# Optimization experiments

Hardware: AMD Instinct MI355X
Metric: run time of the kernel (lower is better)

Reference implementation:

```python
import jax, jax.numpy as jnp
import numpy as np

N = 2048        # nodes
IN_DIM = 128    # input feature dim
K = 8           # channels
D = 32          # per-channel dim (C_dim)
ITERS = 4       # routing iterations
BETA = 1.0      # attention temperature
EPS = 1e-12     # F.normalize eps


def l2norm(x):
    # F.normalize(x, dim=-1): x / max(||x||_2, eps)
    n = jnp.linalg.norm(x, axis=-1, keepdims=True)
    return x / jnp.maximum(n, EPS)


def setup_inputs() -> dict:
    key = jax.random.key(0)
    k1, k2, k3, k4 = jax.random.split(key, 4)
    adj = jax.random.randint(k1, (N, N), 0, 2, dtype=jnp.int32)
    features = jax.random.normal(k2, (N, IN_DIM), dtype=jnp.float32)
    # parameters initialized ~ N(0,1) as in init_parameters
    W = jax.random.normal(k3, (K, IN_DIM, D), dtype=jnp.float32)
    b = jax.random.normal(k4, (K, D), dtype=jnp.float32)
    return {"adj": adj, "features": features, "W": W, "b": b}


def reference(adj, features, W, b):
    mask = (adj > 0)[None, :, :]                         # [1, N, N]
    # per-channel projection + row L2 normalize -> Z: [K, N, D]
    Z = l2norm(jnp.einsum('nd,kdc->knc', features, W) + b[:, None, :])
    for _ in range(ITERS):
        # per-channel masked attention scores [K, N, N]
        att = jnp.einsum('knc,kmc->knm', Z, Z)
        att = jnp.where(mask, att, 0.0) / BETA
        # softmax across channels (dim=2 in torch after cat == K axis here)
        att = jax.nn.softmax(att, axis=0)
        att = jnp.where(mask, att, 0.0)
        # weighted aggregate + residual + L2 normalize
        Z = l2norm(Z + jnp.einsum('knm,kmc->knc', att, Z))
    # concat channels along feature dim -> [N, K*D]
    return jnp.transpose(Z, (1, 0, 2)).reshape(N, K * D)
```

## Files before the change

kernel.cpp:

```cpp
#include <hip/hip_runtime.h>
#include <hip/hip_bf16.h>
#include <hip/hip_fp16.h>
#include <hip/hip_cooperative_groups.h>

namespace cg = cooperative_groups;

#define NN 2048
#define KK 8
#define DD 32
#define ZSZ (KK * NN * DD)

#define TW(row, slot) (((row) << 4) + ((((slot) ^ (((row) >> 1) & 3))) << 2))
#define TW2(row, wo) (((row) << 4) + (((((wo) >> 2) ^ (((row) >> 1) & 3))) << 2) + ((wo) & 3))

typedef __attribute__((ext_vector_type(8))) short short8;
typedef __attribute__((ext_vector_type(4))) short short4v;
typedef __attribute__((ext_vector_type(4))) float f32x4;
typedef __attribute__((ext_vector_type(4))) unsigned int u32x4;

union UU { u32x4 q; short8 v; unsigned int u[4]; };
union U2 { uint2 q; short4v v; unsigned int u[2]; };

__device__ __forceinline__ unsigned int bfr(float x) {
  unsigned int u = __float_as_uint(x);
  return (u + 0x7fffu + ((u >> 16) & 1u)) >> 16;
}
__device__ __forceinline__ float bf2f(unsigned int h) {
  return __uint_as_float(h << 16);
}
__device__ __forceinline__ unsigned int packp(float a, float b) {
  union { __hip_bfloat162 h; unsigned int u; } cv;
  cv.h = __float22bfloat162_rn(make_float2(a, b));
  return cv.u;
}
__device__ __forceinline__ f32x4 MF(short8 a, short8 b, f32x4 c) {
  return __builtin_amdgcn_mfma_f32_16x16x32_bf16(a, b, c, 0, 0, 0);
}
__device__ __forceinline__ f32x4 MF16(short4v a, short4v b, f32x4 c) {
  return __builtin_amdgcn_mfma_f32_16x16x16bf16_1k(a, b, c, 0, 0, 0);
}
__device__ __forceinline__ short8 as_s8(u32x4 x) { UU u; u.q = x; return u.v; }

__global__ __launch_bounds__(256, 2) void mega_kernel(
    const float* feat, const float* W, const float* bias, const int* adj,
    unsigned short* Zghi, unsigned short* Zthi, unsigned int* mbits,
    __half* part, float* out) {
  __shared__ __align__(16) unsigned int lds[20480];
  cg::grid_group grid = cg::this_grid();
  const int bx = blockIdx.x;
  const int t = threadIdx.x;
  const int w = t >> 6;
  const int lane = t & 63;
  const int l15 = lane & 15;
  const int g = lane >> 4;

  unsigned int* Zg = (unsigned int*)Zghi;
  unsigned int* Zt = (unsigned int*)Zthi;

  {
    const int nb = bx * 4;
    const int k = t >> 5, c = t & 31;
    float* fsh = (float*)lds;
    if (t < 128) *(float4*)&fsh[4 * t] = *(const float4*)&feat[nb * 128 + 4 * t];
    float s[4];
#pragma unroll
    for (int j = 0; j < 4; ++j) s[j] = bias[k * DD + c];
    __syncthreads();
    const float* wp = W + (k * 128) * DD + c;
#pragma unroll 4
    for (int d = 0; d < 128; ++d) {
      float wv = wp[d * DD];
#pragma unroll
      for (int j = 0; j < 4; ++j) s[j] = fmaf(fsh[j * 128 + d], wv, s[j]);
    }
    unsigned int hi[4];
#pragma unroll
    for (int j = 0; j < 4; ++j) {
      float sq = s[j] * s[j];
#pragma unroll
      for (int off = 16; off > 0; off >>= 1) sq += __shfl_xor(sq, off, 32);
      float z = s[j] / fmaxf(sqrtf(sq), 1e-12f);
      hi[j] = bfr(z);
      Zghi[(k * NN + nb + j) * DD + c] = (unsigned short)hi[j];
    }
    *(uint2*)&Zthi[(size_t)k * DD * NN + (size_t)c * NN + nb] =
        make_uint2(hi[0] | (hi[1] << 16), hi[2] | (hi[3] << 16));

    const int base = bx * 8192 + t;
#pragma unroll
    for (int q = 0; q < 4; ++q) {
      int v[8];
#pragma unroll
      for (int r = 0; r < 8; ++r) v[r] = adj[base + 256 * (8 * q + r)];
#pragma unroll
      for (int r = 0; r < 8; ++r) {
        int idx = base + 256 * (8 * q + r);
        unsigned long long b = __ballot(v[r] > 0);
        if (lane == 0) mbits[idx >> 5] = (unsigned int)b;
        if (lane == 32) mbits[idx >> 5] = (unsigned int)(b >> 32);
      }
    }
  }
  grid.sync();

  const int nblk = (bx >> 3) & 31;
  const int chunk = (bx & 7) * 2 + (bx >> 8);
  const int nw = nblk * 64 + w * 16;
  const int mchunk = chunk * 128;
  const int sqd = t & 3;
  const int sr0 = t >> 2;

#pragma unroll 1
  for (int it = 0; it < 4; ++it) {
    {
      short8 A[KK];
#pragma unroll
      for (int k = 0; k < KK; ++k)
        A[k] = as_s8(*(const u32x4*)&Zg[(size_t)(k * NN + nw + l15) * 16 + 4 * g]);

      unsigned int mword[4];
      {
        uint4 m4 = *(const uint4*)&mbits[(size_t)(nw + l15) * 64 + (mchunk >> 5)];
        mword[0] = m4.x; mword[1] = m4.y; mword[2] = m4.z; mword[3] = m4.w;
      }

      f32x4 O[KK][2];
#pragma unroll
      for (int k = 0; k < KK; ++k)
#pragma unroll
        for (int ch = 0; ch < 2; ++ch) O[k][ch] = {0.0f, 0.0f, 0.0f, 0.0f};

      u32x4 Lgh[4], Lth[4];
      auto dl_g = [&](int mb) {
#pragma unroll
        for (int j = 0; j < 4; ++j) {
          int r = 64 * j + sr0;
          int k = r >> 5, rm = r & 31;
          Lgh[j] = *(const u32x4*)&Zg[(size_t)(k * NN + mb + rm) * 16 + 4 * sqd];
        }
      };
      auto wr_g = [&](int buf) {
#pragma unroll
        for (int j = 0; j < 4; ++j)
          *(u32x4*)&lds[buf * 4096 + TW(64 * j + sr0, sqd)] = Lgh[j];
      };
      auto dl_t = [&](int mb) {
#pragma unroll
        for (int j = 0; j < 4; ++j) {
          int r = 64 * j + sr0;
          int k = r >> 5, rm = r & 31;
          Lth[j] = *(const u32x4*)&Zt[(size_t)k * (NN * 16) + (size_t)rm * (NN / 2) + (mb >> 1) + 4 * sqd];
        }
      };
      auto wr_t = [&](int buf) {
#pragma unroll
        for (int j = 0; j < 4; ++j)
          *(u32x4*)&lds[12288 + buf * 4096 + TW(64 * j + sr0, sqd)] = Lth[j];
      };
      auto gram = [&](int gbuf, int sub, f32x4* S) {
#pragma unroll
        for (int k = 0; k < KK; ++k) {
          u32x4 bh = *(const u32x4*)&lds[gbuf * 4096 + TW(k * 32 + 16 * sub + l15, g)];
          f32x4 z = {0.0f, 0.0f, 0.0f, 0.0f};
          S[k] = MF(as_s8(bh), A[k], z);
        }
      };
      auto finish = [&](f32x4* S, int tbuf, int sub, unsigned int mw) {
#pragma unroll
        for (int r = 0; r < 4; ++r) {
          float e[KK];
          float sum = 0.0f;
#pragma unroll
          for (int k = 0; k < KK; ++k) { e[k] = __expf(S[k][r]); sum += e[k]; }
          float f = ((mw >> (16 * sub + 4 * g + r)) & 1u) ? __builtin_amdgcn_rcpf(sum) : 0.0f;
#pragma unroll
          for (int k = 0; k < KK; ++k) S[k][r] = e[k] * f;
        }
#pragma unroll
        for (int k = 0; k < KK; ++k) {
          U2 pa;
          pa.u[0] = packp(S[k][0], S[k][1]);
          pa.u[1] = packp(S[k][2], S[k][3]);
#pragma unroll
          for (int ch = 0; ch < 2; ++ch) {
            int row = k * 32 + 16 * ch + l15;
            U2 bv;
            bv.q = *(const uint2*)&lds[12288 + tbuf * 4096 + TW2(row, 8 * sub + 2 * g)];
            O[k][ch] = MF16(pa.v, bv.v, O[k][ch]);
          }
        }
      };

      dl_g(mchunk); wr_g(0);
      dl_g(mchunk + 32); wr_g(1);
      dl_t(mchunk); wr_t(0);
      dl_g(mchunk + 64);
      dl_t(mchunk + 32);
      __syncthreads();

      f32x4 Scur[KK], Snxt[KK];
      gram(0, 0, Scur);

#pragma unroll
      for (int st = 0; st < 4; ++st) {
        if (st + 2 < 4) wr_g((st + 2) % 3);
        if (st + 1 < 4) wr_t((st + 1) & 1);
        if (st + 3 < 4) dl_g(mchunk + (st + 3) * 32);
        if (st + 2 < 4) dl_t(mchunk + (st + 2) * 32);
        const unsigned int mw = mword[st];

        gram(st % 3, 1, Snxt);
        finish(Scur, st & 1, 0, mw);
        if (st + 1 < 4) gram((st + 1) % 3, 0, Scur);
        finish(Snxt, st & 1, 1, mw);
        __syncthreads();
      }

      __half* dst = part + (size_t)chunk * ZSZ;
#pragma unroll
      for (int k = 0; k < KK; ++k)
#pragma unroll
        for (int ch = 0; ch < 2; ++ch) {
          f32x4 o = O[k][ch];
#pragma unroll
          for (int r = 0; r < 4; ++r)
            dst[(size_t)(k * NN + nw + 4 * g + r) * DD + 16 * ch + l15] = __float2half_rn(o[r]);
        }
    }
    grid.sync();

    if (it < 3) {
      {
        unsigned int* T32 = lds;
        const int k = bx >> 6, mt = bx & 63;
        const int m0 = mt * 32;
        const int mloc = t >> 3, c4 = t & 7;
        const size_t idx = (size_t)(k * NN + m0 + mloc) * DD + 4 * c4;
        uint2 zb = *(const uint2*)&Zghi[idx];
        float4 v;
        v.x = bf2f(zb.x & 0xffffu);
        v.y = __uint_as_float(zb.x & 0xffff0000u);
        v.z = bf2f(zb.y & 0xffffu);
        v.w = __uint_as_float(zb.y & 0xffff0000u);
#pragma unroll
        for (int j = 0; j < 16; ++j) {
          const __half2* ph = (const __half2*)&part[(size_t)j * ZSZ + idx];
          float2 a = __half22float2(ph[0]);
          float2 bb = __half22float2(ph[1]);
          v.x += a.x; v.y += a.y; v.z += bb.x; v.w += bb.y;
        }
        float sq = v.x * v.x + v.y * v.y + v.z * v.z + v.w * v.w;
        sq += __shfl_xor(sq, 1, 8);
        sq += __shfl_xor(sq, 2, 8);
        sq += __shfl_xor(sq, 4, 8);
        const float sc = 1.0f / fmaxf(sqrtf(sq), 1e-12f);
        float z[4] = {v.x * sc, v.y * sc, v.z * sc, v.w * sc};
        unsigned int hi[4];
#pragma unroll
        for (int e = 0; e < 4; ++e) {
          hi[e] = bfr(z[e]);
          T32[(4 * c4 + e) * 37 + mloc] = hi[e];
        }
        *(uint2*)&Zghi[idx] = make_uint2(hi[0] | (hi[1] << 16), hi[2] | (hi[3] << 16));
        __syncthreads();
        const int cloc = t >> 3, m4i = t & 7;
        unsigned int o0 = T32[cloc * 37 + 4 * m4i + 0] | (T32[cloc * 37 + 4 * m4i + 1] << 16);
        unsigned int o1 = T32[cloc * 37 + 4 * m4i + 2] | (T32[cloc * 37 + 4 * m4i + 3] << 16);
        *(uint2*)&Zthi[(size_t)k * DD * NN + (size_t)cloc * NN + m0 + 4 * m4i] =
            make_uint2(o0, o1);
        __syncthreads();
      }
      grid.sync();
    }
  }

  {
    const int k = t >> 5, c = t & 31;
#pragma unroll
    for (int jj = 0; jj < 4; ++jj) {
      const int n = bx * 4 + jj;
      const size_t idx = (size_t)(k * NN + n) * DD + c;
      float v = bf2f((unsigned int)Zghi[idx]);
#pragma unroll
      for (int j = 0; j < 16; ++j) v += __half2float(part[(size_t)j * ZSZ + idx]);
      float sq = v * v;
#pragma unroll
      for (int off = 16; off > 0; off >>= 1) sq += __shfl_xor(sq, off, 32);
      out[n * (KK * DD) + t] = v / fmaxf(sqrtf(sq), 1e-12f);
    }
  }
}

__global__ __launch_bounds__(256) void pm_kernel(const float* __restrict__ feat,
                                                 const float* __restrict__ W,
                                                 const float* __restrict__ bias,
                                                 unsigned short* __restrict__ Zghi,
                                                 unsigned short* __restrict__ Zthi,
                                                 const int* __restrict__ adj,
                                                 unsigned int* __restrict__ mbits) {
  __shared__ float fsh[1024];
  const int t = threadIdx.x;
  if (blockIdx.x < 256) {
    const int nb = blockIdx.x * 8;
    const int k = t >> 5, c = t & 31;
    *(float4*)&fsh[4 * t] = *(const float4*)&feat[nb * 128 + 4 * t];
    float s[8];
#pragma unroll
    for (int j = 0; j < 8; ++j) s[j] = bias[k * DD + c];
    const float* w = W + (k * 128) * DD + c;
    __syncthreads();
#pragma unroll 4
    for (int d = 0; d < 128; ++d) {
      float wv = w[d * DD];
#pragma unroll
      for (int j = 0; j < 8; ++j) s[j] = fmaf(fsh[j * 128 + d], wv, s[j]);
    }
    unsigned int hi[8];
#pragma unroll
    for (int j = 0; j < 8; ++j) {
      float sq = s[j] * s[j];
#pragma unroll
      for (int off = 16; off > 0; off >>= 1) sq += __shfl_xor(sq, off, 32);
      float z = s[j] / fmaxf(sqrtf(sq), 1e-12f);
      hi[j] = bfr(z);
      Zghi[(k * NN + nb + j) * DD + c] = (unsigned short)hi[j];
    }
    uint4 tp = make_uint4(hi[0] | (hi[1] << 16), hi[2] | (hi[3] << 16),
                          hi[4] | (hi[5] << 16), hi[6] | (hi[7] << 16));
    *(uint4*)&Zthi[(size_t)k * DD * NN + (size_t)c * NN + nb] = tp;
  } else {
    const int base = (blockIdx.x - 256) * 1024 + t;
    const int lane = t & 63;
    int v[4];
#pragma unroll
    for (int rr = 0; rr < 4; ++rr) v[rr] = adj[base + 256 * rr];
#pragma unroll
    for (int rr = 0; rr < 4; ++rr) {
      int idx = base + 256 * rr;
      unsigned long long b = __ballot(v[rr] > 0);
      if (lane == 0) mbits[idx >> 5] = (unsigned int)b;
      if (lane == 32) mbits[idx >> 5] = (unsigned int)(b >> 32);
    }
  }
}

__global__ __launch_bounds__(256) void rp_kernel(const __half* __restrict__ part,
                                                 unsigned short* __restrict__ Zghi,
                                                 unsigned short* __restrict__ Zthi) {
  __shared__ unsigned int T32[32 * 37];
  const int t = threadIdx.x;
  const int k = blockIdx.x >> 6, mt = blockIdx.x & 63;
  const int m0 = mt * 32;
  const int mloc = t >> 3, c4 = t & 7;
  const size_t idx = (size_t)(k * NN + m0 + mloc) * DD + 4 * c4;
  uint2 zb = *(const uint2*)&Zghi[idx];
  float4 v;
  v.x = bf2f(zb.x & 0xffffu);
  v.y = __uint_as_float(zb.x & 0xffff0000u);
  v.z = bf2f(zb.y & 0xffffu);
  v.w = __uint_as_float(zb.y & 0xffff0000u);
#pragma unroll
  for (int j = 0; j < 16; ++j) {
    const __half2* ph = (const __half2*)&part[(size_t)j * ZSZ + idx];
    float2 a = __half22float2(ph[0]);
    float2 b = __half22float2(ph[1]);
    v.x += a.x; v.y += a.y; v.z += b.x; v.w += b.y;
  }
  float sq = v.x * v.x + v.y * v.y + v.z * v.z + v.w * v.w;
  sq += __shfl_xor(sq, 1, 8);
  sq += __shfl_xor(sq, 2, 8);
  sq += __shfl_xor(sq, 4, 8);
  const float sc = 1.0f / fmaxf(sqrtf(sq), 1e-12f);
  float z[4] = {v.x * sc, v.y * sc, v.z * sc, v.w * sc};
  unsigned int hi[4];
#pragma unroll
  for (int e = 0; e < 4; ++e) {
    hi[e] = bfr(z[e]);
    T32[(4 * c4 + e) * 37 + mloc] = hi[e];
  }
  *(uint2*)&Zghi[idx] = make_uint2(hi[0] | (hi[1] << 16), hi[2] | (hi[3] << 16));
  __syncthreads();
  const int cloc = t >> 3, m4 = t & 7;
  unsigned int o0 = T32[cloc * 37 + 4 * m4 + 0] | (T32[cloc * 37 + 4 * m4 + 1] << 16);
  unsigned int o1 = T32[cloc * 37 + 4 * m4 + 2] | (T32[cloc * 37 + 4 * m4 + 3] << 16);
  *(uint2*)&Zthi[(size_t)k * DD * NN + (size_t)cloc * NN + m0 + 4 * m4] = make_uint2(o0, o1);
}

__global__ __launch_bounds__(256, 2) void iter_kernel(const unsigned short* __restrict__ Zghi,
                                                      const unsigned short* __restrict__ Zthi,
                                                      const unsigned int* __restrict__ mbits,
                                                      __half* __restrict__ part) {
  __shared__ __align__(16) unsigned int lds[20480];
  const int t = threadIdx.x;
  const int w = t >> 6;
  const int lane = t & 63;
  const int l15 = lane & 15;
  const int g = lane >> 4;
  const int bx = blockIdx.x;
  const int nblk = (bx >> 3) & 31;
  const int chunk = (bx & 7) * 2 + (bx >> 8);
  const int nw = nblk * 64 + w * 16;
  const int mchunk = chunk * 128;

  const unsigned int* Zg = (const unsigned int*)Zghi;
  const unsigned int* Zt = (const unsigned int*)Zthi;

  short8 A[KK];
#pragma unroll
  for (int k = 0; k < KK; ++k)
    A[k] = as_s8(*(const u32x4*)&Zg[(size_t)(k * NN + nw + l15) * 16 + 4 * g]);

  unsigned int mword[4];
  {
    uint4 m4 = *(const uint4*)&mbits[(size_t)(nw + l15) * 64 + (mchunk >> 5)];
    mword[0] = m4.x; mword[1] = m4.y; mword[2] = m4.z; mword[3] = m4.w;
  }

  f32x4 O[KK][2];
#pragma unroll
  for (int k = 0; k < KK; ++k)
#pragma unroll
    for (int ch = 0; ch < 2; ++ch) O[k][ch] = {0.0f, 0.0f, 0.0f, 0.0f};

  const int sqd = t & 3;
  const int sr0 = t >> 2;

  u32x4 Lgh[4], Lth[4];
  auto dl_g = [&](int mb) {
#pragma unroll
    for (int j = 0; j < 4; ++j) {
      int r = 64 * j + sr0;
      int k = r >> 5, rm = r & 31;
      Lgh[j] = *(const u32x4*)&Zg[(size_t)(k * NN + mb + rm) * 16 + 4 * sqd];
    }
  };
  auto wr_g = [&](int buf) {
#pragma unroll
    for (int j = 0; j < 4; ++j)
      *(u32x4*)&lds[buf * 4096 + TW(64 * j + sr0, sqd)] = Lgh[j];
  };
  auto dl_t = [&](int mb) {
#pragma unroll
    for (int j = 0; j < 4; ++j) {
      int r = 64 * j + sr0;
      int k = r >> 5, rm = r & 31;
      Lth[j] = *(const u32x4*)&Zt[(size_t)k * (NN * 16) + (size_t)rm * (NN / 2) + (mb >> 1) + 4 * sqd];
    }
  };
  auto wr_t = [&](int buf) {
#pragma unroll
    for (int j = 0; j < 4; ++j)
      *(u32x4*)&lds[12288 + buf * 4096 + TW(64 * j + sr0, sqd)] = Lth[j];
  };
  auto gram = [&](int gbuf, int sub, f32x4* S) {
#pragma unroll
    for (int k = 0; k < KK; ++k) {
      u32x4 bh = *(const u32x4*)&lds[gbuf * 4096 + TW(k * 32 + 16 * sub + l15, g)];
      f32x4 z = {0.0f, 0.0f, 0.0f, 0.0f};
      S[k] = MF(as_s8(bh), A[k], z);
    }
  };
  auto finish = [&](f32x4* S, int tbuf, int sub, unsigned int mw) {
#pragma unroll
    for (int r = 0; r < 4; ++r) {
      float e[KK];
      float sum = 0.0f;
#pragma unroll
      for (int k = 0; k < KK; ++k) { e[k] = __expf(S[k][r]); sum += e[k]; }
      float f = ((mw >> (16 * sub + 4 * g + r)) & 1u) ? __builtin_amdgcn_rcpf(sum) : 0.0f;
#pragma unroll
      for (int k = 0; k < KK; ++k) S[k][r] = e[k] * f;
    }
#pragma unroll
    for (int k = 0; k < KK; ++k) {
      U2 pa;
      pa.u[0] = packp(S[k][0], S[k][1]);
      pa.u[1] = packp(S[k][2], S[k][3]);
#pragma unroll
      for (int ch = 0; ch < 2; ++ch) {
        int row = k * 32 + 16 * ch + l15;
        U2 bv;
        bv.q = *(const uint2*)&lds[12288 + tbuf * 4096 + TW2(row, 8 * sub + 2 * g)];
        O[k][ch] = MF16(pa.v, bv.v, O[k][ch]);
      }
    }
  };

  dl_g(mchunk); wr_g(0);
  dl_g(mchunk + 32); wr_g(1);
  dl_t(mchunk); wr_t(0);
  dl_g(mchunk + 64);
  dl_t(mchunk + 32);
  __syncthreads();

  f32x4 Scur[KK], Snxt[KK];
  gram(0, 0, Scur);

#pragma unroll
  for (int st = 0; st < 4; ++st) {
    if (st + 2 < 4) wr_g((st + 2) % 3);
    if (st + 1 < 4) wr_t((st + 1) & 1);
    if (st + 3 < 4) dl_g(mchunk + (st + 3) * 32);
    if (st + 2 < 4) dl_t(mchunk + (st + 2) * 32);
    const unsigned int mw = mword[st];

    gram(st % 3, 1, Snxt);
    finish(Scur, st & 1, 0, mw);
    if (st + 1 < 4) gram((st + 1) % 3, 0, Scur);
    finish(Snxt, st & 1, 1, mw);
    __syncthreads();
  }

  __half* dst = part + (size_t)chunk * ZSZ;
#pragma unroll
  for (int k = 0; k < KK; ++k)
#pragma unroll
    for (int ch = 0; ch < 2; ++ch) {
      f32x4 o = O[k][ch];
#pragma unroll
      for (int r = 0; r < 4; ++r)
        dst[(size_t)(k * NN + nw + 4 * g + r) * DD + 16 * ch + l15] = __float2half_rn(o[r]);
    }
}

__global__ __launch_bounds__(256) void ro_kernel(const unsigned short* __restrict__ Zghi,
                                                 const __half* __restrict__ part,
                                                 float* __restrict__ out) {
  const int n = blockIdx.x, t = threadIdx.x;
  const int k = t >> 5, c = t & 31;
  const size_t idx = (size_t)(k * NN + n) * DD + c;
  float v = bf2f((unsigned int)Zghi[idx]);
#pragma unroll
  for (int j = 0; j < 16; ++j) v += __half2float(part[(size_t)j * ZSZ + idx]);
  float sq = v * v;
#pragma unroll
  for (int off = 16; off > 0; off >>= 1) sq += __shfl_xor(sq, off, 32);
  out[n * (KK * DD) + t] = v / fmaxf(sqrtf(sq), 1e-12f);
}

extern "C" void kernel_launch(void* const* d_in, const int* in_sizes, int n_in,
                              void* d_out, int out_size, void* d_ws, size_t ws_size,
                              hipStream_t stream) {
  const int* adj = (const int*)d_in[0];
  const float* feat = (const float*)d_in[1];
  const float* W = (const float*)d_in[2];
  const float* b = (const float*)d_in[3];
  float* out = (float*)d_out;

  unsigned short* Zghi = (unsigned short*)d_ws;
  unsigned short* Zthi = Zghi + ZSZ;
  unsigned int* mbits = (unsigned int*)(Zthi + ZSZ);
  __half* part = (__half*)(mbits + NN * 64);

  bool coop_ok = false;
  int maxb = 0;
  if (hipOccupancyMaxActiveBlocksPerMultiprocessor(&maxb, mega_kernel, 256, 0) == hipSuccess &&
      maxb >= 2) {
    void* kargs[] = {(void*)&feat, (void*)&W, (void*)&b, (void*)&adj,
                     (void*)&Zghi, (void*)&Zthi, (void*)&mbits, (void*)&part, (void*)&out};
    if (hipLaunchCooperativeKernel((const void*)mega_kernel, dim3(512), dim3(256), kargs, 0,
                                   stream) == hipSuccess)
      coop_ok = true;
  }
  if (coop_ok) return;

  pm_kernel<<<256 + 4096, 256, 0, stream>>>(feat, W, b, Zghi, Zthi, adj, mbits);
  for (int it = 0; it < 4; ++it) {
    iter_kernel<<<512, 256, 0, stream>>>(Zghi, Zthi, mbits, part);
    if (it < 3)
      rp_kernel<<<512, 256, 0, stream>>>(part, Zghi, Zthi);
    else
      ro_kernel<<<NN, 256, 0, stream>>>(Zghi, part, out);
  }
}
```

Baseline: 182.1 us.

## Permute transposed Z layout so one 16-byte LDS read serves both sub-tiles

```diff
diff --git a/kernel.cpp b/kernel.cpp
--- a/kernel.cpp
+++ b/kernel.cpp
@@ -11,7 +11,6 @@
 #define ZSZ (KK * NN * DD)
 
 #define TW(row, slot) (((row) << 4) + ((((slot) ^ (((row) >> 1) & 3))) << 2))
-#define TW2(row, wo) (((row) << 4) + (((((wo) >> 2) ^ (((row) >> 1) & 3))) << 2) + ((wo) & 3))
 
 typedef __attribute__((ext_vector_type(8))) short short8;
 typedef __attribute__((ext_vector_type(4))) short short4v;
@@ -40,6 +39,7 @@
   return __builtin_amdgcn_mfma_f32_16x16x16bf16_1k(a, b, c, 0, 0, 0);
 }
 __device__ __forceinline__ short8 as_s8(u32x4 x) { UU u; u.q = x; return u.v; }
+
 
 __global__ __launch_bounds__(256, 2) void mega_kernel(
     const float* feat, const float* W, const float* bias, const int* adj,
@@ -83,8 +83,13 @@
       hi[j] = bfr(z);
       Zghi[(k * NN + nb + j) * DD + c] = (unsigned short)hi[j];
     }
-    *(uint2*)&Zthi[(size_t)k * DD * NN + (size_t)c * NN + nb] =
-        make_uint2(hi[0] | (hi[1] << 16), hi[2] | (hi[3] << 16));
+    {
+      const size_t base = ((size_t)k * DD * NN + (size_t)c * NN) >> 1;
+      const int v = bx & 7;
+      const int p0 = 4 * (v & 3) + 2 * (v >> 2);
+      *(uint2*)&Zt[base + (size_t)(bx >> 3) * 16 + p0] =
+          make_uint2(hi[0] | (hi[1] << 16), hi[2] | (hi[3] << 16));
+    }
 
     const int base = bx * 8192 + t;
 #pragma unroll
@@ -130,6 +135,8 @@
 #pragma unroll
         for (int ch = 0; ch < 2; ++ch) O[k][ch] = {0.0f, 0.0f, 0.0f, 0.0f};
 
+      uint2 Bhi[KK][2];
+
       u32x4 Lgh[4], Lth[4];
       auto dl_g = [&](int mb) {
 #pragma unroll
@@ -165,14 +172,14 @@
           S[k] = MF(as_s8(bh), A[k], z);
         }
       };
-      auto finish = [&](f32x4* S, int tbuf, int sub, unsigned int mw) {
+      auto finish0 = [&](f32x4* S, int tbuf, unsigned int mw) {
 #pragma unroll
         for (int r = 0; r < 4; ++r) {
           float e[KK];
           float sum = 0.0f;
 #pragma unroll
           for (int k = 0; k < KK; ++k) { e[k] = __expf(S[k][r]); sum += e[k]; }
-          float f = ((mw >> (16 * sub + 4 * g + r)) & 1u) ? __builtin_amdgcn_rcpf(sum) : 0.0f;
+          float f = ((mw >> (4 * g + r)) & 1u) ? __builtin_amdgcn_rcpf(sum) : 0.0f;
 #pragma unroll
           for (int k = 0; k < KK; ++k) S[k][r] = e[k] * f;
         }
@@ -184,8 +191,32 @@
 #pragma unroll
           for (int ch = 0; ch < 2; ++ch) {
             int row = k * 32 + 16 * ch + l15;
-            U2 bv;
-            bv.q = *(const uint2*)&lds[12288 + tbuf * 4096 + TW2(row, 8 * sub + 2 * g)];
+            u32x4 q = *(const u32x4*)&lds[12288 + tbuf * 4096 + TW(row, g)];
+            U2 bv; bv.u[0] = q.x; bv.u[1] = q.y;
+            Bhi[k][ch] = make_uint2(q.z, q.w);
+            O[k][ch] = MF16(pa.v, bv.v, O[k][ch]);
+          }
+        }
+      };
+      auto finish1 = [&](f32x4* S, unsigned int mw) {
+#pragma unroll
+        for (int r = 0; r < 4; ++r) {
+          float e[KK];
+          float sum = 0.0f;
+#pragma unroll
+          for (int k = 0; k < KK; ++k) { e[k] = __expf(S[k][r]); sum += e[k]; }
+          float f = ((mw >> (16 + 4 * g + r)) & 1u) ? __builtin_amdgcn_rcpf(sum) : 0.0f;
+#pragma unroll
+          for (int k = 0; k < KK; ++k) S[k][r] = e[k] * f;
+        }
+#pragma unroll
+        for (int k = 0; k < KK; ++k) {
+          U2 pa;
+          pa.u[0] = packp(S[k][0], S[k][1]);
+          pa.u[1] = packp(S[k][2], S[k][3]);
+#pragma unroll
+          for (int ch = 0; ch < 2; ++ch) {
+            U2 bv; bv.u[0] = Bhi[k][ch].x; bv.u[1] = Bhi[k][ch].y;
             O[k][ch] = MF16(pa.v, bv.v, O[k][ch]);
           }
         }
@@ -210,9 +241,9 @@
         const unsigned int mw = mword[st];
 
         gram(st % 3, 1, Snxt);
-        finish(Scur, st & 1, 0, mw);
+        finish0(Scur, st & 1, mw);
         if (st + 1 < 4) gram((st + 1) % 3, 0, Scur);
-        finish(Snxt, st & 1, 1, mw);
+        finish1(Snxt, mw);
         __syncthreads();
       }
 
@@ -266,8 +297,9 @@
         const int cloc = t >> 3, m4i = t & 7;
         unsigned int o0 = T32[cloc * 37 + 4 * m4i + 0] | (T32[cloc * 37 + 4 * m4i + 1] << 16);
         unsigned int o1 = T32[cloc * 37 + 4 * m4i + 2] | (T32[cloc * 37 + 4 * m4i + 3] << 16);
-        *(uint2*)&Zthi[(size_t)k * DD * NN + (size_t)cloc * NN + m0 + 4 * m4i] =
-            make_uint2(o0, o1);
+        const size_t base = ((size_t)k * DD * NN + (size_t)cloc * NN) >> 1;
+        const int p0 = 4 * (m4i & 3) + 2 * (m4i >> 2);
+        *(uint2*)&Zt[base + (size_t)(m0 >> 1) + p0] = make_uint2(o0, o1);
         __syncthreads();
       }
       grid.sync();
@@ -325,9 +357,13 @@
       hi[j] = bfr(z);
       Zghi[(k * NN + nb + j) * DD + c] = (unsigned short)hi[j];
     }
-    uint4 tp = make_uint4(hi[0] | (hi[1] << 16), hi[2] | (hi[3] << 16),
-                          hi[4] | (hi[5] << 16), hi[6] | (hi[7] << 16));
-    *(uint4*)&Zthi[(size_t)k * DD * NN + (size_t)c * NN + nb] = tp;
+    unsigned int* Zt = (unsigned int*)Zthi;
+    const size_t base = ((size_t)k * DD * NN + (size_t)c * NN) >> 1;
+    const int w0 = (nb >> 1) & 15;
+    const int p0 = 4 * ((w0 >> 1) & 3) + 2 * (w0 >> 3);
+    const size_t gb = base + (size_t)(nb >> 5) * 16;
+    *(uint2*)&Zt[gb + p0] = make_uint2(hi[0] | (hi[1] << 16), hi[2] | (hi[3] << 16));
+    *(uint2*)&Zt[gb + p0 + 4] = make_uint2(hi[4] | (hi[5] << 16), hi[6] | (hi[7] << 16));
   } else {
     const int base = (blockIdx.x - 256) * 1024 + t;
     const int lane = t & 63;
@@ -383,7 +419,10 @@
   const int cloc = t >> 3, m4 = t & 7;
   unsigned int o0 = T32[cloc * 37 + 4 * m4 + 0] | (T32[cloc * 37 + 4 * m4 + 1] << 16);
   unsigned int o1 = T32[cloc * 37 + 4 * m4 + 2] | (T32[cloc * 37 + 4 * m4 + 3] << 16);
-  *(uint2*)&Zthi[(size_t)k * DD * NN + (size_t)cloc * NN + m0 + 4 * m4] = make_uint2(o0, o1);
+  unsigned int* Zt = (unsigned int*)Zthi;
+  const size_t base = ((size_t)k * DD * NN + (size_t)cloc * NN) >> 1;
+  const int p0 = 4 * (m4 & 3) + 2 * (m4 >> 2);
+  *(uint2*)&Zt[base + (size_t)(m0 >> 1) + p0] = make_uint2(o0, o1);
 }
 
 __global__ __launch_bounds__(256, 2) void iter_kernel(const unsigned short* __restrict__ Zghi,
@@ -422,6 +461,8 @@
 #pragma unroll
     for (int ch = 0; ch < 2; ++ch) O[k][ch] = {0.0f, 0.0f, 0.0f, 0.0f};
 
+  uint2 Bhi[KK][2];
+
   const int sqd = t & 3;
   const int sr0 = t >> 2;
 
@@ -460,14 +501,14 @@
       S[k] = MF(as_s8(bh), A[k], z);
     }
   };
-  auto finish = [&](f32x4* S, int tbuf, int sub, unsigned int mw) {
+  auto finish0 = [&](f32x4* S, int tbuf, unsigned int mw) {
 #pragma unroll
     for (int r = 0; r < 4; ++r) {
       float e[KK];
       float sum = 0.0f;
 #pragma unroll
       for (int k = 0; k < KK; ++k) { e[k] = __expf(S[k][r]); sum += e[k]; }
-      float f = ((mw >> (16 * sub + 4 * g + r)) & 1u) ? __builtin_amdgcn_rcpf(sum) : 0.0f;
+      float f = ((mw >> (4 * g + r)) & 1u) ? __builtin_amdgcn_rcpf(sum) : 0.0f;
 #pragma unroll
       for (int k = 0; k < KK; ++k) S[k][r] = e[k] * f;
     }
@@ -479,8 +520,32 @@
 #pragma unroll
       for (int ch = 0; ch < 2; ++ch) {
         int row = k * 32 + 16 * ch + l15;
-        U2 bv;
-        bv.q = *(const uint2*)&lds[12288 + tbuf * 4096 + TW2(row, 8 * sub + 2 * g)];
+        u32x4 q = *(const u32x4*)&lds[12288 + tbuf * 4096 + TW(row, g)];
+        U2 bv; bv.u[0] = q.x; bv.u[1] = q.y;
+        Bhi[k][ch] = make_uint2(q.z, q.w);
+        O[k][ch] = MF16(pa.v, bv.v, O[k][ch]);
+      }
+    }
+  };
+  auto finish1 = [&](f32x4* S, unsigned int mw) {
+#pragma unroll
+    for (int r = 0; r < 4; ++r) {
+      float e[KK];
+      float sum = 0.0f;
+#pragma unroll
+      for (int k = 0; k < KK; ++k) { e[k] = __expf(S[k][r]); sum += e[k]; }
+      float f = ((mw >> (16 + 4 * g + r)) & 1u) ? __builtin_amdgcn_rcpf(sum) : 0.0f;
+#pragma unroll
+      for (int k = 0; k < KK; ++k) S[k][r] = e[k] * f;
+    }
+#pragma unroll
+    for (int k = 0; k < KK; ++k) {
+      U2 pa;
+      pa.u[0] = packp(S[k][0], S[k][1]);
+      pa.u[1] = packp(S[k][2], S[k][3]);
+#pragma unroll
+      for (int ch = 0; ch < 2; ++ch) {
+        U2 bv; bv.u[0] = Bhi[k][ch].x; bv.u[1] = Bhi[k][ch].y;
         O[k][ch] = MF16(pa.v, bv.v, O[k][ch]);
       }
     }
@@ -505,9 +570,9 @@
     const unsigned int mw = mword[st];
 
     gram(st % 3, 1, Snxt);
-    finish(Scur, st & 1, 0, mw);
+    finish0(Scur, st & 1, mw);
     if (st + 1 < 4) gram((st + 1) % 3, 0, Scur);
-    finish(Snxt, st & 1, 1, mw);
+    finish1(Snxt, mw);
     __syncthreads();
   }
 
```

After: 195.3 us. 1.07x slower.
